# Kernel optimization log

Measured on AMD Instinct MI355X. Metric: run time of the kernel, lower is better.

## Reference

```python
import jax, jax.numpy as jnp
import numpy as np

SPATIAL_W = 1.0
FREQ_W = 1.0
CONTRASTIVE_W = 0.5
TEMPERATURE = 0.07

B, D = 8192, 256
N_SCENES = 4096


def setup_inputs() -> dict:
    key = jax.random.key(0)
    k1, k2, k3 = jax.random.split(key, 3)
    clean_features = jax.random.normal(k1, (B, D), dtype=jnp.float32)
    turb_features = jax.random.normal(k2, (B, D), dtype=jnp.float32)
    # integer scene ids stand in for the filename strings (only equality is used)
    scene_ids = jax.random.randint(k3, (B,), 0, N_SCENES, dtype=jnp.int64)
    return {"clean_features": clean_features, "turb_features": turb_features,
            "scene_ids": scene_ids}


def _l2_normalize(x, eps=1e-12):
    # matches F.normalize(x, dim=1): x / max(||x||, eps)
    n = jnp.linalg.norm(x, axis=1, keepdims=True)
    return x / jnp.maximum(n, eps)


def reference(clean_features, turb_features, scene_ids):
    # 1) spatial invariance: MSE over (B, D)
    spatial = jnp.mean((clean_features - turb_features) ** 2)

    # 2) frequency consistency: MSE of rfft magnitudes along feature dim
    clean_mag = jnp.abs(jnp.fft.rfft(clean_features, axis=1))
    turb_mag = jnp.abs(jnp.fft.rfft(turb_features, axis=1))
    frequency = jnp.mean((clean_mag - turb_mag) ** 2)

    # 3) InfoNCE-style contrastive with filename-equality positives
    cn = _l2_normalize(clean_features)
    tn = _l2_normalize(turb_features)
    sim = jnp.einsum('id,jd->ij', cn, tn) / TEMPERATURE      # (B, B)
    labels = (scene_ids[:, None] == scene_ids[None, :]).astype(sim.dtype)
    exp_sim = jnp.exp(sim)
    positive_sum = jnp.sum(exp_sim * labels, axis=1)
    all_sum = jnp.sum(exp_sim, axis=1)
    contrastive = jnp.mean(-jnp.log(positive_sum / (all_sum + 1e-8)))

    total = SPATIAL_W * spatial + FREQ_W * frequency + CONTRASTIVE_W * contrastive
    return jnp.stack([total, spatial, frequency, contrastive])
```

## Files before the change

### kernel.cpp

```cpp
#include <hip/hip_runtime.h>

#define NROWS 8192
#define DDIM  256
#define NBINS 129

typedef float f32x4 __attribute__((ext_vector_type(4)));
typedef short bf16x8 __attribute__((ext_vector_type(8)));

__device__ __forceinline__ float wave_red(float v) {
#pragma unroll
    for (int m = 32; m; m >>= 1) v += __shfl_xor(v, m, 64);
    return v;
}

__device__ __forceinline__ unsigned bfbits(float f) {
    union { float f; unsigned u; } v; v.f = f;
    return (v.u + 0x7FFFu + ((v.u >> 16) & 1u)) >> 16;
}

__device__ __forceinline__ void gload_lds16(const void* g, void* l) {
    __builtin_amdgcn_global_load_lds((const __attribute__((address_space(1))) void*)g,
                                     (__attribute__((address_space(3))) void*)l,
                                     16, 0, 0);
}

__global__ __launch_bounds__(256) void k_basis(unsigned short* __restrict__ basisT) {
    const int n = blockIdx.x;
    const int k = threadIdx.x;
    float v = 0.0f;
    const float step = 0.0245436926f;
    if (n < 129)                  v = cosf(step * (float)((n * k) & 255));
    else if (n >= 144 && n < 273) v = sinf(step * (float)(((n - 144) * k) & 255));
    basisT[n * DDIM + k] = (unsigned short)bfbits(v);
}

__global__ __launch_bounds__(256) void k_prep(const float* __restrict__ clean,
                                              const float* __restrict__ turb,
                                              const unsigned short* __restrict__ basisT,
                                              unsigned short* __restrict__ cnb,
                                              unsigned short* __restrict__ tnb,
                                              float* __restrict__ spat_part,
                                              float* __restrict__ freq_part) {
    __shared__ unsigned short xn[2][16][264];
    __shared__ float nrm[16][2];
    __shared__ float sp4[4], rbuf[4];

    const int t    = threadIdx.x;
    const int w    = t >> 6;
    const int lane = t & 63;
    const int rb   = blockIdx.x * 16;

    float4 xc4[4], xt4[4];
    float dsq = 0.0f;
#pragma unroll
    for (int q = 0; q < 4; ++q) {
        const int row = q * 4 + w;
        const float* pc = clean + (rb + row) * DDIM + lane * 4;
        const float* pt = turb  + (rb + row) * DDIM + lane * 4;
        xc4[q] = *(const float4*)pc;
        xt4[q] = *(const float4*)pt;
        const float4 a = xc4[q], b = xt4[q];
        dsq += (a.x - b.x) * (a.x - b.x) + (a.y - b.y) * (a.y - b.y)
             + (a.z - b.z) * (a.z - b.z) + (a.w - b.w) * (a.w - b.w);
        float nsc = a.x * a.x + a.y * a.y + a.z * a.z + a.w * a.w;
        float nst = b.x * b.x + b.y * b.y + b.z * b.z + b.w * b.w;
        nsc = wave_red(nsc);
        nst = wave_red(nst);
        if (lane == 0) {
            nrm[row][0] = fmaxf(sqrtf(nsc), 1e-12f);
            nrm[row][1] = fmaxf(sqrtf(nst), 1e-12f);
        }
    }
    dsq = wave_red(dsq);
    if (lane == 0) sp4[w] = dsq;
    __syncthreads();

#pragma unroll
    for (int q = 0; q < 4; ++q) {
        const int row = q * 4 + w;
        const float ic = 1.0f / nrm[row][0], it = 1.0f / nrm[row][1];
        const float4 a = xc4[q], b = xt4[q];
        uint2 pc, pt;
        pc.x = bfbits(a.x * ic) | (bfbits(a.y * ic) << 16);
        pc.y = bfbits(a.z * ic) | (bfbits(a.w * ic) << 16);
        pt.x = bfbits(b.x * it) | (bfbits(b.y * it) << 16);
        pt.y = bfbits(b.z * it) | (bfbits(b.w * it) << 16);
        *(uint2*)(cnb + (rb + row) * DDIM + lane * 4) = pc;
        *(uint2*)(tnb + (rb + row) * DDIM + lane * 4) = pt;
        *(uint2*)&xn[0][row][lane * 4] = pc;
        *(uint2*)&xn[1][row][lane * 4] = pt;
    }
    __syncthreads();

    const int fr = lane & 15;
    const int fc = (lane >> 4) << 3;
    bf16x8 ac[8], at[8];
#pragma unroll
    for (int kk = 0; kk < 8; ++kk) {
        ac[kk] = *(const bf16x8*)&xn[0][fr][fc + kk * 32];
        at[kk] = *(const bf16x8*)&xn[1][fr][fc + kk * 32];
    }

    const int lrow = (lane >> 4) << 2;
    float nc4[4], nt4[4];
#pragma unroll
    for (int r = 0; r < 4; ++r) {
        nc4[r] = nrm[lrow + r][0];
        nt4[r] = nrm[lrow + r][1];
    }

    const int nlo = (w == 0) ? 0 : (w * 2 + 1);
    const int nhi = (w == 0) ? 3 : (w * 2 + 3);
    const unsigned short* bcb = basisT + fr * DDIM + fc;
    const unsigned short* bsb = basisT + (144 + fr) * DDIM + fc;

    float fsum = 0.0f;
#pragma unroll 1
    for (int n = nlo; n < nhi; ++n) {
        f32x4 acc_cc = (f32x4){0.f, 0.f, 0.f, 0.f};
        f32x4 acc_cs = (f32x4){0.f, 0.f, 0.f, 0.f};
        f32x4 acc_tc = (f32x4){0.f, 0.f, 0.f, 0.f};
        f32x4 acc_ts = (f32x4){0.f, 0.f, 0.f, 0.f};
#pragma unroll
        for (int kk = 0; kk < 8; ++kk) {
            const bf16x8 bc = *(const bf16x8*)(bcb + n * 16 * DDIM + kk * 32);
            const bf16x8 bs = *(const bf16x8*)(bsb + n * 16 * DDIM + kk * 32);
            acc_cc = __builtin_amdgcn_mfma_f32_16x16x32_bf16(ac[kk], bc, acc_cc, 0, 0, 0);
            acc_tc = __builtin_amdgcn_mfma_f32_16x16x32_bf16(at[kk], bc, acc_tc, 0, 0, 0);
            acc_cs = __builtin_amdgcn_mfma_f32_16x16x32_bf16(ac[kk], bs, acc_cs, 0, 0, 0);
            acc_ts = __builtin_amdgcn_mfma_f32_16x16x32_bf16(at[kk], bs, acc_ts, 0, 0, 0);
        }
#pragma unroll
        for (int r = 0; r < 4; ++r) {
            const float mc = nc4[r] * sqrtf(acc_cc[r] * acc_cc[r] + acc_cs[r] * acc_cs[r]);
            const float mt = nt4[r] * sqrtf(acc_tc[r] * acc_tc[r] + acc_ts[r] * acc_ts[r]);
            const float d = mc - mt;
            fsum += d * d;
        }
    }
    fsum = wave_red(fsum);
    if (lane == 0) rbuf[w] = fsum;
    __syncthreads();
    if (t == 0) {
        freq_part[blockIdx.x] = rbuf[0] + rbuf[1] + rbuf[2] + rbuf[3];
        spat_part[blockIdx.x] = sp4[0] + sp4[1] + sp4[2] + sp4[3];
    }
}

#define BM 128
#define BN 128
#define BK 64

__global__ __launch_bounds__(256) void k_gemm(const unsigned short* __restrict__ cnb,
                                              const unsigned short* __restrict__ tnb,
                                              const int* __restrict__ sid,
                                              float* __restrict__ pall,
                                              float* __restrict__ ppos) {
    __shared__ unsigned short As[BM][BK];
    __shared__ unsigned short Bs[BN][BK];
    __shared__ float ps[2][BM][2];
    __shared__ int sidI[BM], sidJ[BN];

    const int bid = blockIdx.x;
    const int xcd = bid & 7;
    const int q   = bid >> 3;
    const int grp = q >> 6;
    const int r   = q & 63;
    const int ib  = xcd * 8 + (r >> 3);
    const int jb  = grp * 8 + (r & 7);
    const int i0  = ib * BM;
    const int j0  = jb * BN;

    const int t = threadIdx.x;
    if (t < 128) sidI[t] = sid[i0 + t];
    else         sidJ[t - 128] = sid[j0 + t - 128];

    const int wid  = t >> 6;
    const int lane = t & 63;
    const int wrow = (wid >> 1) * 64;
    const int wcol = (wid & 1) * 64;
    const int rx   = lane & 7;

    f32x4 acc[4][4];
#pragma unroll
    for (int m = 0; m < 4; ++m)
#pragma unroll
        for (int n = 0; n < 4; ++n)
            acc[m][n] = (f32x4){0.f, 0.f, 0.f, 0.f};

    for (int kt = 0; kt < DDIM / BK; ++kt) {
#pragma unroll
        for (int it = 0; it < 4; ++it) {
            const int g  = it * 256 + t;
            const int rr = g >> 3;
            const int sl = g & 7;
            const int sc = ((sl ^ (rr & 7)) << 3);
            gload_lds16(cnb + (i0 + rr) * DDIM + kt * BK + sc,
                        (char*)&As[0][0] + g * 16);
            gload_lds16(tnb + (j0 + rr) * DDIM + kt * BK + sc,
                        (char*)&Bs[0][0] + g * 16);
        }
        __syncthreads();
#pragma unroll
        for (int kk = 0; kk < BK / 32; ++kk) {
            const int kslot = kk * 4 + (lane >> 4);
            bf16x8 af[4], bfr[4];
#pragma unroll
            for (int m = 0; m < 4; ++m) {
                const int row = wrow + m * 16 + (lane & 15);
                af[m] = *(const bf16x8*)((const char*)&As[0][0]
                          + row * 128 + ((kslot ^ rx) << 4));
            }
#pragma unroll
            for (int n = 0; n < 4; ++n) {
                const int row = wcol + n * 16 + (lane & 15);
                bfr[n] = *(const bf16x8*)((const char*)&Bs[0][0]
                          + row * 128 + ((kslot ^ rx) << 4));
            }
#pragma unroll
            for (int m = 0; m < 4; ++m)
#pragma unroll
                for (int n = 0; n < 4; ++n)
                    acc[m][n] = __builtin_amdgcn_mfma_f32_16x16x32_bf16(
                        bfr[n], af[m], acc[m][n], 0, 0, 0);
        }
        __syncthreads();
    }

    const float C = (1.0f / 0.07f) * 1.442695041f;
#pragma unroll
    for (int m = 0; m < 4; ++m) {
        const int rowm = wrow + m * 16 + (lane & 15);
        const int si = sidI[rowm];
        float ra = 0.0f, rp = 0.0f;
#pragma unroll
        for (int n = 0; n < 4; ++n) {
            const int cb = wcol + n * 16 + ((lane >> 4) << 2);
            const int4 sj4 = *(const int4*)&sidJ[cb];
            float e0 = exp2f(acc[m][n][0] * C);
            float e1 = exp2f(acc[m][n][1] * C);
            float e2 = exp2f(acc[m][n][2] * C);
            float e3 = exp2f(acc[m][n][3] * C);
            ra += e0 + e1 + e2 + e3;
            rp += (si == sj4.x) ? e0 : 0.0f;
            rp += (si == sj4.y) ? e1 : 0.0f;
            rp += (si == sj4.z) ? e2 : 0.0f;
            rp += (si == sj4.w) ? e3 : 0.0f;
        }
        ra += __shfl_xor(ra, 16, 64);
        ra += __shfl_xor(ra, 32, 64);
        rp += __shfl_xor(rp, 16, 64);
        rp += __shfl_xor(rp, 32, 64);
        if (lane < 16) {
            ps[wid & 1][wrow + m * 16 + lane][0] = ra;
            ps[wid & 1][wrow + m * 16 + lane][1] = rp;
        }
    }
    __syncthreads();
    if (t < BM) {
        const float sa = ps[0][t][0] + ps[1][t][0];
        const float sp = ps[0][t][1] + ps[1][t][1];
        pall[jb * NROWS + i0 + t] = sa;
        ppos[jb * NROWS + i0 + t] = sp;
    }
}

__global__ __launch_bounds__(256) void k_red(const float* __restrict__ pall,
                                             const float* __restrict__ ppos,
                                             float* __restrict__ contrib) {
    __shared__ float red[256];
    const int row = blockIdx.x * 256 + threadIdx.x;
    float sa = 0.0f, sp = 0.0f;
    for (int jb = 0; jb < 64; ++jb) {
        sa += pall[jb * NROWS + row];
        sp += ppos[jb * NROWS + row];
    }
    red[threadIdx.x] = logf(sa + 1e-8f) - logf(sp);
    __syncthreads();
#pragma unroll
    for (int s = 128; s > 0; s >>= 1) {
        if (threadIdx.x < s) red[threadIdx.x] += red[threadIdx.x + s];
        __syncthreads();
    }
    if (threadIdx.x == 0) contrib[blockIdx.x] = red[0];
}

__global__ __launch_bounds__(256) void k_final(const float* __restrict__ spat_part,
                                               const float* __restrict__ freq_part,
                                               const float* __restrict__ contrib,
                                               float* __restrict__ out) {
    __shared__ float reda[256], redb[256], redc[256];
    float a = 0.0f, b = 0.0f, c = 0.0f;
    for (int i = threadIdx.x; i < 512; i += 256) {
        a += spat_part[i];
        b += freq_part[i];
    }
    if (threadIdx.x < 32) c = contrib[threadIdx.x];
    reda[threadIdx.x] = a; redb[threadIdx.x] = b; redc[threadIdx.x] = c;
    __syncthreads();
#pragma unroll
    for (int s = 128; s > 0; s >>= 1) {
        if (threadIdx.x < s) {
            reda[threadIdx.x] += reda[threadIdx.x + s];
            redb[threadIdx.x] += redb[threadIdx.x + s];
            redc[threadIdx.x] += redc[threadIdx.x + s];
        }
        __syncthreads();
    }
    if (threadIdx.x == 0) {
        float spatial = reda[0] / (float)(NROWS * DDIM);
        float frequency = redb[0] / (float)(NROWS * NBINS);
        float contrastive = redc[0] / (float)NROWS;
        out[0] = spatial + frequency + 0.5f * contrastive;
        out[1] = spatial;
        out[2] = frequency;
        out[3] = contrastive;
    }
}

extern "C" void kernel_launch(void* const* d_in, const int* in_sizes, int n_in,
                              void* d_out, int out_size, void* d_ws, size_t ws_size,
                              hipStream_t stream) {
    const float* clean = (const float*)d_in[0];
    const float* turb  = (const float*)d_in[1];
    const int*   sids  = (const int*)d_in[2];

    char* ws = (char*)d_ws;
    unsigned short* cnb    = (unsigned short*)ws;
    unsigned short* tnb    = (unsigned short*)(ws + 4194304);
    unsigned short* basisT = (unsigned short*)(ws + 8388608);
    float* pall      = (float*)(ws + 8650752);
    float* ppos      = (float*)(ws + 10747904);
    float* spat_part = (float*)(ws + 12845056);
    float* freq_part = (float*)(ws + 12849152);
    float* contrib   = (float*)(ws + 12853248);

    hipLaunchKernelGGL(k_basis, dim3(288), dim3(256), 0, stream, basisT);
    hipLaunchKernelGGL(k_prep, dim3(NROWS / 16), dim3(256), 0, stream,
                       clean, turb, basisT, cnb, tnb, spat_part, freq_part);
    hipLaunchKernelGGL(k_gemm, dim3(4096), dim3(256), 0, stream,
                       cnb, tnb, sids, pall, ppos);
    hipLaunchKernelGGL(k_red, dim3(NROWS / 256), dim3(256), 0, stream,
                       pall, ppos, contrib);
    hipLaunchKernelGGL(k_final, dim3(1), dim3(256), 0, stream,
                       spat_part, freq_part, contrib, (float*)d_out);
}
```

Measured before the change: 86.78 us.

## Quantize normalized features to FP8 and run similarity GEMM with FP8 MFMA

The prep kernel now writes the L2-normalized clean and turbulent features as FP8 (scaled by 16) instead of bf16. The similarity GEMM loads 128-byte K tiles and uses the fp8 16x16x32 MFMA, and the exp scale constant is adjusted to undo the 256x product scaling. This halves the operand bytes and K-loop iterations and uses the higher-throughput FP8 matrix path. The cost is reduced precision in similarity logits, which the exp/temperature amplify and may push the contrastive loss outside tolerance.

```diff
diff --git a/kernel.cpp b/kernel.cpp
--- a/kernel.cpp
+++ b/kernel.cpp
@@ -37,8 +37,8 @@
 __global__ __launch_bounds__(256) void k_prep(const float* __restrict__ clean,
                                               const float* __restrict__ turb,
                                               const unsigned short* __restrict__ basisT,
-                                              unsigned short* __restrict__ cnb,
-                                              unsigned short* __restrict__ tnb,
+                                              unsigned char* __restrict__ cnb,
+                                              unsigned char* __restrict__ tnb,
                                               float* __restrict__ spat_part,
                                               float* __restrict__ freq_part) {
     __shared__ unsigned short xn[2][16][264];
@@ -78,17 +78,23 @@
 #pragma unroll
     for (int q = 0; q < 4; ++q) {
         const int row = q * 4 + w;
-        const float ic = 1.0f / nrm[row][0], it = 1.0f / nrm[row][1];
+        const float icb = 1.0f / nrm[row][0], itb = 1.0f / nrm[row][1];
+        const float icq = 16.0f * icb, itq = 16.0f * itb;
         const float4 a = xc4[q], b = xt4[q];
         uint2 pc, pt;
-        pc.x = bfbits(a.x * ic) | (bfbits(a.y * ic) << 16);
-        pc.y = bfbits(a.z * ic) | (bfbits(a.w * ic) << 16);
-        pt.x = bfbits(b.x * it) | (bfbits(b.y * it) << 16);
-        pt.y = bfbits(b.z * it) | (bfbits(b.w * it) << 16);
-        *(uint2*)(cnb + (rb + row) * DDIM + lane * 4) = pc;
-        *(uint2*)(tnb + (rb + row) * DDIM + lane * 4) = pt;
+        pc.x = bfbits(a.x * icb) | (bfbits(a.y * icb) << 16);
+        pc.y = bfbits(a.z * icb) | (bfbits(a.w * icb) << 16);
+        pt.x = bfbits(b.x * itb) | (bfbits(b.y * itb) << 16);
+        pt.y = bfbits(b.z * itb) | (bfbits(b.w * itb) << 16);
         *(uint2*)&xn[0][row][lane * 4] = pc;
         *(uint2*)&xn[1][row][lane * 4] = pt;
+        int f8c = 0, f8t = 0;
+        f8c = __builtin_amdgcn_cvt_pk_fp8_f32(a.x * icq, a.y * icq, f8c, false);
+        f8c = __builtin_amdgcn_cvt_pk_fp8_f32(a.z * icq, a.w * icq, f8c, true);
+        f8t = __builtin_amdgcn_cvt_pk_fp8_f32(b.x * itq, b.y * itq, f8t, false);
+        f8t = __builtin_amdgcn_cvt_pk_fp8_f32(b.z * itq, b.w * itq, f8t, true);
+        *(int*)(cnb + (rb + row) * DDIM + lane * 4) = f8c;
+        *(int*)(tnb + (rb + row) * DDIM + lane * 4) = f8t;
     }
     __syncthreads();
 
@@ -149,15 +155,15 @@
 
 #define BM 128
 #define BN 128
-#define BK 64
-
-__global__ __launch_bounds__(256) void k_gemm(const unsigned short* __restrict__ cnb,
-                                              const unsigned short* __restrict__ tnb,
+#define BKF 128
+
+__global__ __launch_bounds__(256) void k_gemm(const unsigned char* __restrict__ cnb,
+                                              const unsigned char* __restrict__ tnb,
                                               const int* __restrict__ sid,
                                               float* __restrict__ pall,
                                               float* __restrict__ ppos) {
-    __shared__ unsigned short As[BM][BK];
-    __shared__ unsigned short Bs[BN][BK];
+    __shared__ unsigned char As[BM][BKF];
+    __shared__ unsigned char Bs[BN][BKF];
     __shared__ float ps[2][BM][2];
     __shared__ int sidI[BM], sidJ[BN];
 
@@ -188,46 +194,48 @@
         for (int n = 0; n < 4; ++n)
             acc[m][n] = (f32x4){0.f, 0.f, 0.f, 0.f};
 
-    for (int kt = 0; kt < DDIM / BK; ++kt) {
+    for (int kt = 0; kt < DDIM / BKF; ++kt) {
 #pragma unroll
         for (int it = 0; it < 4; ++it) {
             const int g  = it * 256 + t;
             const int rr = g >> 3;
             const int sl = g & 7;
-            const int sc = ((sl ^ (rr & 7)) << 3);
-            gload_lds16(cnb + (i0 + rr) * DDIM + kt * BK + sc,
+            const int sc = (sl ^ (rr & 7)) << 4;
+            gload_lds16(cnb + (i0 + rr) * DDIM + kt * BKF + sc,
                         (char*)&As[0][0] + g * 16);
-            gload_lds16(tnb + (j0 + rr) * DDIM + kt * BK + sc,
+            gload_lds16(tnb + (j0 + rr) * DDIM + kt * BKF + sc,
                         (char*)&Bs[0][0] + g * 16);
         }
         __syncthreads();
 #pragma unroll
-        for (int kk = 0; kk < BK / 32; ++kk) {
-            const int kslot = kk * 4 + (lane >> 4);
-            bf16x8 af[4], bfr[4];
+        for (int kk = 0; kk < 4; ++kk) {
+            const int bb   = kk * 32 + ((lane >> 4) << 3);
+            const int gcol = bb >> 4;
+            const int boff = bb & 15;
+            long af[4], bfr[4];
 #pragma unroll
             for (int m = 0; m < 4; ++m) {
                 const int row = wrow + m * 16 + (lane & 15);
-                af[m] = *(const bf16x8*)((const char*)&As[0][0]
-                          + row * 128 + ((kslot ^ rx) << 4));
+                af[m] = *(const long*)((const char*)&As[0][0]
+                          + row * BKF + ((gcol ^ rx) << 4) + boff);
             }
 #pragma unroll
             for (int n = 0; n < 4; ++n) {
                 const int row = wcol + n * 16 + (lane & 15);
-                bfr[n] = *(const bf16x8*)((const char*)&Bs[0][0]
-                          + row * 128 + ((kslot ^ rx) << 4));
+                bfr[n] = *(const long*)((const char*)&Bs[0][0]
+                          + row * BKF + ((gcol ^ rx) << 4) + boff);
             }
 #pragma unroll
             for (int m = 0; m < 4; ++m)
 #pragma unroll
                 for (int n = 0; n < 4; ++n)
-                    acc[m][n] = __builtin_amdgcn_mfma_f32_16x16x32_bf16(
+                    acc[m][n] = __builtin_amdgcn_mfma_f32_16x16x32_fp8_fp8(
                         bfr[n], af[m], acc[m][n], 0, 0, 0);
         }
         __syncthreads();
     }
 
-    const float C = (1.0f / 0.07f) * 1.442695041f;
+    const float C = 1.442695041f / (0.07f * 256.0f);
 #pragma unroll
     for (int m = 0; m < 4; ++m) {
         const int rowm = wrow + m * 16 + (lane & 15);
@@ -326,8 +334,8 @@
     const int*   sids  = (const int*)d_in[2];
 
     char* ws = (char*)d_ws;
-    unsigned short* cnb    = (unsigned short*)ws;
-    unsigned short* tnb    = (unsigned short*)(ws + 4194304);
+    unsigned char* cnb     = (unsigned char*)ws;
+    unsigned char* tnb     = (unsigned char*)(ws + 4194304);
     unsigned short* basisT = (unsigned short*)(ws + 8388608);
     float* pall      = (float*)(ws + 8650752);
     float* ppos      = (float*)(ws + 10747904);
```

Result: faster. 75.62 us (-12.9%).
